# Kernel optimization log

Hardware: AMD Instinct MI355X
Metric: run time of the kernel (lower is better)

The kernel has to match this reference:

```python
import jax, jax.numpy as jnp
import numpy as np

NEG_INF = -1.0e9
VALID_THRESH = -1.0e8
EPS = 1e-12


def _l2_normalize(x):
    n = jnp.linalg.norm(x, axis=-1, keepdims=True)
    return x / jnp.maximum(n, EPS)


def setup_inputs() -> dict:
    key = jax.random.key(0)
    k1, k2, k3, k4 = jax.random.split(key, 4)
    B, Nq, Nd, D = 64, 32, 256, 128
    return {
        "query_embeds": jax.random.normal(k1, (B, Nq, D), dtype=jnp.float32),
        "query_mask": jax.random.randint(k2, (B, Nq), 0, 2, dtype=jnp.int32),
        "doc_embeds": jax.random.normal(k3, (B, Nd, D), dtype=jnp.float32),
        "doc_mask": jax.random.randint(k4, (B, Nd), 0, 2, dtype=jnp.int32),
    }


def reference(query_embeds, query_mask, doc_embeds, doc_mask):
    # normalize=True, symmetric=True path
    q = _l2_normalize(query_embeds)
    d = _l2_normalize(doc_embeds)
    qm = query_mask.astype(jnp.float32)[..., None]  # [B, Nq, 1]
    dm = doc_mask.astype(jnp.float32)[..., None]    # [B, Nd, 1]
    q = q * qm
    d = d * dm

    # token_sims: [Bq, Bd, Nq, Nd]
    token_sims = jnp.einsum("qtd,csd->qcts", q, d)
    # pair mask: [Bq,1,Nq,1] * [1,Bd,1,Nd]
    mask = qm[:, None, :, :] * dm[None, :, :, 0][:, :, None, :].transpose(1, 0, 2, 3)
    masked_sims = jnp.where(mask > 0, token_sims, NEG_INF)

    # query -> doc max over doc tokens
    q2d = jnp.max(masked_sims, axis=-1)          # [Bq, Bd, Nq]
    valid_q = (q2d > VALID_THRESH).astype(jnp.float32)
    q2d = jnp.where(valid_q > 0, q2d, 0.0)
    cnt_q = jnp.maximum(jnp.sum(valid_q, axis=-1), 1.0)
    q2d_score = jnp.sum(q2d, axis=-1) / cnt_q    # [Bq, Bd]

    # doc -> query max over query tokens
    d2q = jnp.max(masked_sims, axis=-2)          # [Bq, Bd, Nd]
    valid_d = (d2q > VALID_THRESH).astype(jnp.float32)
    d2q = jnp.where(valid_d > 0, d2q, 0.0)
    cnt_d = jnp.maximum(jnp.sum(valid_d, axis=-1), 1.0)
    d2q_score = jnp.sum(d2q, axis=-1) / cnt_d    # [Bq, Bd]

    return (q2d_score + d2q_score) / 2.0
```

## Files before the change

kernel.cpp:

```cpp
#include <hip/hip_runtime.h>
#include <hip/hip_bf16.h>

typedef short bf16x8 __attribute__((ext_vector_type(8)));
typedef short short8 __attribute__((ext_vector_type(8)));
typedef float f32x4 __attribute__((ext_vector_type(4)));

#define B_   64
#define NQ   32
#define ND   256
#define DIM  128
#define MT   4
#define NEG_INF_F (-1.0e9f)
#define VALID_F   (-1.0e8f)

__global__ __launch_bounds__(256) void normalize_rows(
    const float* __restrict__ q, const int* __restrict__ qmask,
    const float* __restrict__ d, const int* __restrict__ dmask,
    __hip_bfloat16* __restrict__ qn, __hip_bfloat16* __restrict__ dn)
{
    const int tid  = threadIdx.x;
    const int sub  = tid & 15;
    const int row  = blockIdx.x * 16 + (tid >> 4);

    const float* src;
    __hip_bfloat16* dst;
    int m;
    if (row < B_ * NQ) {
        src = q + row * DIM;  dst = qn + row * DIM;  m = qmask[row];
    } else {
        const int r2 = row - B_ * NQ;
        src = d + r2 * DIM;   dst = dn + r2 * DIM;   m = dmask[r2];
    }

    const float4 v0 = *reinterpret_cast<const float4*>(src + sub * 8);
    const float4 v1 = *reinterpret_cast<const float4*>(src + sub * 8 + 4);
    float ss = v0.x*v0.x + v0.y*v0.y + v0.z*v0.z + v0.w*v0.w
             + v1.x*v1.x + v1.y*v1.y + v1.z*v1.z + v1.w*v1.w;
    #pragma unroll
    for (int off = 1; off <= 8; off <<= 1) ss += __shfl_xor(ss, off);

    const float scale = m ? (1.0f / fmaxf(sqrtf(ss), 1e-12f)) : 0.0f;

    short8 o;
    const float f[8] = {v0.x, v0.y, v0.z, v0.w, v1.x, v1.y, v1.z, v1.w};
    #pragma unroll
    for (int j = 0; j < 8; ++j) {
        __hip_bfloat16 b = __float2bfloat16(f[j] * scale);
        o[j] = *reinterpret_cast<short*>(&b);
    }
    *reinterpret_cast<short8*>(dst + sub * 8) = o;
}

__global__ __launch_bounds__(256) void chamfer_main(
    const __hip_bfloat16* __restrict__ qn,
    const __hip_bfloat16* __restrict__ dn,
    const int* __restrict__ qmask,
    const int* __restrict__ dmask,
    float* __restrict__ out)
{
    const int bq0 = (blockIdx.x >> 6) * MT;
    const int bd  = blockIdx.x & 63;
    const int tid = threadIdx.x;
    const int w   = tid >> 6;
    const int l   = tid & 63;
    const int lr  = l & 15;
    const int lk  = l >> 4;

    const __hip_bfloat16* Dp = dn + (bd * ND + w * 64) * DIM;

    f32x4 acc[MT][2][4] = {};

    #pragma unroll
    for (int kk = 0; kk < 4; ++kk) {
        const int k0 = kk * 32 + lk * 8;
        bf16x8 bfr[4];
        #pragma unroll
        for (int ni = 0; ni < 4; ++ni)
            bfr[ni] = *reinterpret_cast<const bf16x8*>(Dp + (ni * 16 + lr) * DIM + k0);
        #pragma unroll
        for (int m = 0; m < MT; ++m) {
            const __hip_bfloat16* Q = qn + (bq0 + m) * (NQ * DIM);
            const bf16x8 a0 = *reinterpret_cast<const bf16x8*>(Q + lr * DIM + k0);
            const bf16x8 a1 = *reinterpret_cast<const bf16x8*>(Q + (16 + lr) * DIM + k0);
            #pragma unroll
            for (int ni = 0; ni < 4; ++ni) {
                acc[m][0][ni] = __builtin_amdgcn_mfma_f32_16x16x32_bf16(a0, bfr[ni], acc[m][0][ni], 0, 0, 0);
                acc[m][1][ni] = __builtin_amdgcn_mfma_f32_16x16x32_bf16(a1, bfr[ni], acc[m][1][ni], 0, 0, 0);
            }
        }
    }

    __shared__ float s_rmax[4][MT][NQ];
    __shared__ float s_sd[4][MT], s_cd[4][MT];

    #pragma unroll
    for (int m = 0; m < MT; ++m) {
        const int bq = bq0 + m;
        int qmv[2][4];
        #pragma unroll
        for (int mi = 0; mi < 2; ++mi)
            #pragma unroll
            for (int r = 0; r < 4; ++r)
                qmv[mi][r] = qmask[bq * NQ + mi * 16 + lk * 4 + r];
        int dmv[4];
        #pragma unroll
        for (int ni = 0; ni < 4; ++ni)
            dmv[ni] = dmask[bq * ND + w * 64 + ni * 16 + lr];

        float rmax[2][4];
        float cmax[4];
        #pragma unroll
        for (int ni = 0; ni < 4; ++ni) cmax[ni] = NEG_INF_F;
        #pragma unroll
        for (int mi = 0; mi < 2; ++mi) {
            #pragma unroll
            for (int r = 0; r < 4; ++r) {
                float rm = NEG_INF_F;
                #pragma unroll
                for (int ni = 0; ni < 4; ++ni) {
                    const float v = (qmv[mi][r] && dmv[ni]) ? acc[m][mi][ni][r] : NEG_INF_F;
                    rm = fmaxf(rm, v);
                    cmax[ni] = fmaxf(cmax[ni], v);
                }
                rmax[mi][r] = rm;
            }
        }

        #pragma unroll
        for (int ni = 0; ni < 4; ++ni) {
            cmax[ni] = fmaxf(cmax[ni], __shfl_xor(cmax[ni], 16));
            cmax[ni] = fmaxf(cmax[ni], __shfl_xor(cmax[ni], 32));
        }
        float sd = 0.0f, cd = 0.0f;
        if (lk == 0) {
            #pragma unroll
            for (int ni = 0; ni < 4; ++ni)
                if (cmax[ni] > VALID_F) { sd += cmax[ni]; cd += 1.0f; }
        }
        #pragma unroll
        for (int off = 1; off <= 32; off <<= 1) {
            sd += __shfl_xor(sd, off);
            cd += __shfl_xor(cd, off);
        }
        if (l == 0) { s_sd[w][m] = sd; s_cd[w][m] = cd; }

        #pragma unroll
        for (int mi = 0; mi < 2; ++mi) {
            #pragma unroll
            for (int r = 0; r < 4; ++r) {
                #pragma unroll
                for (int off = 1; off <= 8; off <<= 1)
                    rmax[mi][r] = fmaxf(rmax[mi][r], __shfl_xor(rmax[mi][r], off));
            }
        }
        if (lr == 0) {
            #pragma unroll
            for (int mi = 0; mi < 2; ++mi)
                #pragma unroll
                for (int r = 0; r < 4; ++r)
                    s_rmax[w][m][mi * 16 + lk * 4 + r] = rmax[mi][r];
        }
    }
    __syncthreads();

    {
        const int m = w;
        float v = NEG_INF_F;
        if (l < NQ) {
            #pragma unroll
            for (int wv = 0; wv < 4; ++wv) v = fmaxf(v, s_rmax[wv][m][l]);
        }
        float sq = 0.0f, cq = 0.0f;
        if (l < NQ && v > VALID_F) { sq = v; cq = 1.0f; }
        #pragma unroll
        for (int off = 1; off <= 32; off <<= 1) {
            sq += __shfl_xor(sq, off);
            cq += __shfl_xor(cq, off);
        }
        if (l == 0) {
            const float q2d = sq / fmaxf(cq, 1.0f);
            const float sdt = s_sd[0][m] + s_sd[1][m] + s_sd[2][m] + s_sd[3][m];
            const float cdt = s_cd[0][m] + s_cd[1][m] + s_cd[2][m] + s_cd[3][m];
            const float d2q = sdt / fmaxf(cdt, 1.0f);
            out[(bq0 + m) * B_ + bd] = 0.5f * (q2d + d2q);
        }
    }
}

extern "C" void kernel_launch(void* const* d_in, const int* in_sizes, int n_in,
                              void* d_out, int out_size, void* d_ws, size_t ws_size,
                              hipStream_t stream) {
    const float* q  = (const float*)d_in[0];
    const int*   qm = (const int*)d_in[1];
    const float* d  = (const float*)d_in[2];
    const int*   dm = (const int*)d_in[3];
    float* out = (float*)d_out;

    __hip_bfloat16* qn = (__hip_bfloat16*)d_ws;
    __hip_bfloat16* dn = qn + (B_ * NQ) * DIM;

    normalize_rows<<<(B_ * NQ + B_ * ND) / 16, 256, 0, stream>>>(q, qm, d, dm, qn, dn);
    chamfer_main<<<(B_ / MT) * B_, 256, 0, stream>>>(qn, dn, qm, dm, out);
}
```

Baseline: 115.5 us.

## Stage Q/D tiles into LDS via direct global-to-LDS loads with XOR swizzle

The normalize kernel now writes each bf16 row with an XOR-swizzled 16-byte chunk order. The main kernel copies the whole doc tile and the four query tiles into shared memory using global_load_lds, then reads MFMA operands from LDS at swizzled offsets to avoid bank conflicts. Mask loads are hoisted ahead of the barrier, and the column-max reduction now goes through shared memory. This replaces redundant strided global/L2 operand loads with one coalesced bulk copy, at the cost of about 100KB of LDS per block, which limits occupancy to one block per CU.

```diff
diff --git a/kernel.cpp b/kernel.cpp
--- a/kernel.cpp
+++ b/kernel.cpp
@@ -1,5 +1,6 @@
 #include <hip/hip_runtime.h>
 #include <hip/hip_bf16.h>
+#include <stdint.h>
 
 typedef short bf16x8 __attribute__((ext_vector_type(8)));
 typedef short short8 __attribute__((ext_vector_type(8)));
@@ -12,6 +13,14 @@
 #define MT   4
 #define NEG_INF_F (-1.0e9f)
 #define VALID_F   (-1.0e8f)
+
+
+__device__ __forceinline__ void lds_cp16(const void* g, void* l) {
+    __builtin_amdgcn_global_load_lds(
+        (const __attribute__((address_space(1))) unsigned int*)g,
+        (__attribute__((address_space(3))) unsigned int*)l,
+        16, 0, 0);
+}
 
 __global__ __launch_bounds__(256) void normalize_rows(
     const float* __restrict__ q, const int* __restrict__ qmask,
@@ -24,12 +33,13 @@
 
     const float* src;
     __hip_bfloat16* dst;
-    int m;
+    int m, lrow;
     if (row < B_ * NQ) {
-        src = q + row * DIM;  dst = qn + row * DIM;  m = qmask[row];
+        lrow = row;
+        src = q + (size_t)lrow * DIM;  dst = qn + (size_t)lrow * DIM;  m = qmask[lrow];
     } else {
-        const int r2 = row - B_ * NQ;
-        src = d + r2 * DIM;   dst = dn + r2 * DIM;   m = dmask[r2];
+        lrow = row - B_ * NQ;
+        src = d + (size_t)lrow * DIM;  dst = dn + (size_t)lrow * DIM;  m = dmask[lrow];
     }
 
     const float4 v0 = *reinterpret_cast<const float4*>(src + sub * 8);
@@ -48,7 +58,8 @@
         __hip_bfloat16 b = __float2bfloat16(f[j] * scale);
         o[j] = *reinterpret_cast<short*>(&b);
     }
-    *reinterpret_cast<short8*>(dst + sub * 8) = o;
+    const int chunk = sub ^ (lrow & 7);
+    *reinterpret_cast<short8*>(dst + chunk * 8) = o;
 }
 
 __global__ __launch_bounds__(256) void chamfer_main(
@@ -58,6 +69,11 @@
     const int* __restrict__ dmask,
     float* __restrict__ out)
 {
+    __shared__ __hip_bfloat16 ldsD[ND * DIM];
+    __shared__ __hip_bfloat16 ldsQ[MT * NQ * DIM];
+    __shared__ float s_cmax[MT][ND];
+    __shared__ float s_rmaxT[MT][NQ][4];
+
     const int bq0 = (blockIdx.x >> 6) * MT;
     const int bd  = blockIdx.x & 63;
     const int tid = threadIdx.x;
@@ -66,47 +82,60 @@
     const int lr  = l & 15;
     const int lk  = l >> 4;
 
-    const __hip_bfloat16* Dp = dn + (bd * ND + w * 64) * DIM;
+    {
+        const char* gD = (const char*)(dn + (size_t)(bd * ND) * DIM) + w * 16384;
+        char*       lD = (char*)&ldsD[0] + w * 16384;
+        #pragma unroll
+        for (int c = 0; c < 16; ++c)
+            lds_cp16(gD + c * 1024 + l * 16, lD + c * 1024);
+        const char* gQ = (const char*)(qn + (size_t)(bq0 * NQ) * DIM) + w * 8192;
+        char*       lQ = (char*)&ldsQ[0] + w * 8192;
+        #pragma unroll
+        for (int c = 0; c < 8; ++c)
+            lds_cp16(gQ + c * 1024 + l * 16, lQ + c * 1024);
+    }
+
+    int qmv[MT][2][4];
+    int dmv[MT][4];
+    #pragma unroll
+    for (int m = 0; m < MT; ++m) {
+        #pragma unroll
+        for (int mi = 0; mi < 2; ++mi)
+            #pragma unroll
+            for (int r = 0; r < 4; ++r)
+                qmv[m][mi][r] = qmask[(bq0 + m) * NQ + mi * 16 + lk * 4 + r];
+        #pragma unroll
+        for (int ni = 0; ni < 4; ++ni)
+            dmv[m][ni] = dmask[(bq0 + m) * ND + w * 64 + ni * 16 + lr];
+    }
+
+    __syncthreads();
 
     f32x4 acc[MT][2][4] = {};
-
     #pragma unroll
     for (int kk = 0; kk < 4; ++kk) {
-        const int k0 = kk * 32 + lk * 8;
+        const int slot = (kk * 4 + lk) ^ (lr & 7);
         bf16x8 bfr[4];
         #pragma unroll
-        for (int ni = 0; ni < 4; ++ni)
-            bfr[ni] = *reinterpret_cast<const bf16x8*>(Dp + (ni * 16 + lr) * DIM + k0);
+        for (int ni = 0; ni < 4; ++ni) {
+            const int rowd = w * 64 + ni * 16 + lr;
+            bfr[ni] = *reinterpret_cast<const bf16x8*>((const char*)&ldsD[0] + rowd * 256 + slot * 16);
+        }
         #pragma unroll
         for (int m = 0; m < MT; ++m) {
-            const __hip_bfloat16* Q = qn + (bq0 + m) * (NQ * DIM);
-            const bf16x8 a0 = *reinterpret_cast<const bf16x8*>(Q + lr * DIM + k0);
-            const bf16x8 a1 = *reinterpret_cast<const bf16x8*>(Q + (16 + lr) * DIM + k0);
-            #pragma unroll
-            for (int ni = 0; ni < 4; ++ni) {
-                acc[m][0][ni] = __builtin_amdgcn_mfma_f32_16x16x32_bf16(a0, bfr[ni], acc[m][0][ni], 0, 0, 0);
-                acc[m][1][ni] = __builtin_amdgcn_mfma_f32_16x16x32_bf16(a1, bfr[ni], acc[m][1][ni], 0, 0, 0);
+            #pragma unroll
+            for (int mi = 0; mi < 2; ++mi) {
+                const int rowq = m * NQ + mi * 16 + lr;
+                const bf16x8 a = *reinterpret_cast<const bf16x8*>((const char*)&ldsQ[0] + rowq * 256 + slot * 16);
+                #pragma unroll
+                for (int ni = 0; ni < 4; ++ni)
+                    acc[m][mi][ni] = __builtin_amdgcn_mfma_f32_16x16x32_bf16(a, bfr[ni], acc[m][mi][ni], 0, 0, 0);
             }
         }
     }
 
-    __shared__ float s_rmax[4][MT][NQ];
-    __shared__ float s_sd[4][MT], s_cd[4][MT];
-
     #pragma unroll
     for (int m = 0; m < MT; ++m) {
-        const int bq = bq0 + m;
-        int qmv[2][4];
-        #pragma unroll
-        for (int mi = 0; mi < 2; ++mi)
-            #pragma unroll
-            for (int r = 0; r < 4; ++r)
-                qmv[mi][r] = qmask[bq * NQ + mi * 16 + lk * 4 + r];
-        int dmv[4];
-        #pragma unroll
-        for (int ni = 0; ni < 4; ++ni)
-            dmv[ni] = dmask[bq * ND + w * 64 + ni * 16 + lr];
-
         float rmax[2][4];
         float cmax[4];
         #pragma unroll
@@ -118,70 +147,65 @@
                 float rm = NEG_INF_F;
                 #pragma unroll
                 for (int ni = 0; ni < 4; ++ni) {
-                    const float v = (qmv[mi][r] && dmv[ni]) ? acc[m][mi][ni][r] : NEG_INF_F;
+                    const float v = (qmv[m][mi][r] && dmv[m][ni]) ? acc[m][mi][ni][r] : NEG_INF_F;
                     rm = fmaxf(rm, v);
                     cmax[ni] = fmaxf(cmax[ni], v);
                 }
                 rmax[mi][r] = rm;
             }
         }
-
         #pragma unroll
         for (int ni = 0; ni < 4; ++ni) {
             cmax[ni] = fmaxf(cmax[ni], __shfl_xor(cmax[ni], 16));
             cmax[ni] = fmaxf(cmax[ni], __shfl_xor(cmax[ni], 32));
         }
+        if (lk == 0) {
+            #pragma unroll
+            for (int ni = 0; ni < 4; ++ni)
+                s_cmax[m][w * 64 + ni * 16 + lr] = cmax[ni];
+        }
+        #pragma unroll
+        for (int mi = 0; mi < 2; ++mi)
+            #pragma unroll
+            for (int r = 0; r < 4; ++r) {
+                #pragma unroll
+                for (int off = 1; off <= 8; off <<= 1)
+                    rmax[mi][r] = fmaxf(rmax[mi][r], __shfl_xor(rmax[mi][r], off));
+            }
+        if (lr == 0) {
+            #pragma unroll
+            for (int mi = 0; mi < 2; ++mi)
+                #pragma unroll
+                for (int r = 0; r < 4; ++r)
+                    s_rmaxT[m][mi * 16 + lk * 4 + r][w] = rmax[mi][r];
+        }
+    }
+    __syncthreads();
+
+    {
+        const int m = w;
+        const float4 cm = *reinterpret_cast<const float4*>(&s_cmax[m][l * 4]);
         float sd = 0.0f, cd = 0.0f;
-        if (lk == 0) {
-            #pragma unroll
-            for (int ni = 0; ni < 4; ++ni)
-                if (cmax[ni] > VALID_F) { sd += cmax[ni]; cd += 1.0f; }
+        if (cm.x > VALID_F) { sd += cm.x; cd += 1.0f; }
+        if (cm.y > VALID_F) { sd += cm.y; cd += 1.0f; }
+        if (cm.z > VALID_F) { sd += cm.z; cd += 1.0f; }
+        if (cm.w > VALID_F) { sd += cm.w; cd += 1.0f; }
+        float sq = 0.0f, cq = 0.0f;
+        if (l < NQ) {
+            const float4 rm4 = *reinterpret_cast<const float4*>(&s_rmaxT[m][l][0]);
+            const float v = fmaxf(fmaxf(rm4.x, rm4.y), fmaxf(rm4.z, rm4.w));
+            if (v > VALID_F) { sq = v; cq = 1.0f; }
         }
         #pragma unroll
         for (int off = 1; off <= 32; off <<= 1) {
             sd += __shfl_xor(sd, off);
             cd += __shfl_xor(cd, off);
-        }
-        if (l == 0) { s_sd[w][m] = sd; s_cd[w][m] = cd; }
-
-        #pragma unroll
-        for (int mi = 0; mi < 2; ++mi) {
-            #pragma unroll
-            for (int r = 0; r < 4; ++r) {
-                #pragma unroll
-                for (int off = 1; off <= 8; off <<= 1)
-                    rmax[mi][r] = fmaxf(rmax[mi][r], __shfl_xor(rmax[mi][r], off));
-            }
-        }
-        if (lr == 0) {
-            #pragma unroll
-            for (int mi = 0; mi < 2; ++mi)
-                #pragma unroll
-                for (int r = 0; r < 4; ++r)
-                    s_rmax[w][m][mi * 16 + lk * 4 + r] = rmax[mi][r];
-        }
-    }
-    __syncthreads();
-
-    {
-        const int m = w;
-        float v = NEG_INF_F;
-        if (l < NQ) {
-            #pragma unroll
-            for (int wv = 0; wv < 4; ++wv) v = fmaxf(v, s_rmax[wv][m][l]);
-        }
-        float sq = 0.0f, cq = 0.0f;
-        if (l < NQ && v > VALID_F) { sq = v; cq = 1.0f; }
-        #pragma unroll
-        for (int off = 1; off <= 32; off <<= 1) {
             sq += __shfl_xor(sq, off);
             cq += __shfl_xor(cq, off);
         }
         if (l == 0) {
             const float q2d = sq / fmaxf(cq, 1.0f);
-            const float sdt = s_sd[0][m] + s_sd[1][m] + s_sd[2][m] + s_sd[3][m];
-            const float cdt = s_cd[0][m] + s_cd[1][m] + s_cd[2][m] + s_cd[3][m];
-            const float d2q = sdt / fmaxf(cdt, 1.0f);
+            const float d2q = sd / fmaxf(cd, 1.0f);
             out[(bq0 + m) * B_ + bd] = 0.5f * (q2d + d2q);
         }
     }
```

New measurement: 94.59 us. -18.1%, faster.
